# Kernel optimization log

Measured on AMD Instinct MI355X. Metric: run time of the kernel, lower is better.

## Reference

```python
import jax, jax.numpy as jnp
import numpy as np

NUM_TAGS = 48
START = 46
STOP = 47
B = 1024
S = 512
NEG_INF = -10000.0


def setup_inputs() -> dict:
    key = jax.random.key(0)
    k1, k2, k3, k4 = jax.random.split(key, 4)
    emissions = jax.random.normal(k1, (B, S, NUM_TAGS), dtype=jnp.float32)
    tags = jax.random.randint(k2, (B, S), 0, 46, dtype=jnp.int32)
    lengths = jax.random.randint(k3, (B,), S // 2, S + 1, dtype=jnp.int32)
    mask = (jnp.arange(S, dtype=jnp.int32)[None, :] < lengths[:, None]).astype(jnp.int32)
    # transitions parameter: uniform(-0.1, 0.1), then constraints from reset_parameters
    transitions = jax.random.uniform(k4, (NUM_TAGS, NUM_TAGS), dtype=jnp.float32,
                                     minval=-0.1, maxval=0.1)
    transitions = transitions.at[:, START].set(NEG_INF).at[STOP, :].set(NEG_INF)
    return {"emissions": emissions, "tags": tags, "mask": mask, "transitions": transitions}


def _log_sum_exp(x, axis):
    # matches torch helper: max + log(clamp(sum(exp(x - max)), 1e-10))
    m = jnp.max(x, axis=axis, keepdims=True)
    s = jnp.sum(jnp.exp(x - m), axis=axis, keepdims=True)
    return jnp.squeeze(m + jnp.log(jnp.clip(s, 1e-10)), axis=axis)


def _forward_alg(emissions, transitions, mask):
    b, s, t = emissions.shape
    alpha0 = jnp.full((b, t), NEG_INF, dtype=emissions.dtype).at[:, START].set(0.0)

    def step(alpha, xs):
        emit, m = xs  # emit: (B, T), m: (B,)
        # (B, prev, next)
        nxt = alpha[:, :, None] + transitions[None, :, :] + emit[:, None, :]
        alpha_t = _log_sum_exp(nxt, axis=1)
        alpha = jnp.where(m[:, None] > 0, alpha_t, alpha)
        return alpha, None

    alpha, _ = jax.lax.scan(step, alpha0,
                            (jnp.transpose(emissions, (1, 0, 2)), mask.T))
    terminal = alpha + transitions[STOP][None, :]
    return _log_sum_exp(terminal, axis=1)  # (B,)


def _score_sequence(emissions, transitions, tags, mask):
    b, s, _ = emissions.shape
    start_col = jnp.full((b, 1), START, dtype=tags.dtype)
    tws = jnp.concatenate([start_col, tags], axis=1)  # (B, S+1)
    # transitions[next, prev] per the original _score_sequence
    trans_sc = transitions[tws[:, 1:], tws[:, :-1]]  # (B, S)
    emit_sc = jnp.take_along_axis(emissions, tags[:, :, None].astype(jnp.int32), axis=2)[..., 0]
    score = jnp.sum((trans_sc + emit_sc) * mask.astype(emissions.dtype), axis=1)
    lengths = jnp.sum(mask, axis=1)
    last_tags = jnp.take_along_axis(tags, (lengths - 1)[:, None], axis=1)[:, 0]
    return score + transitions[STOP, last_tags]


def reference(emissions, tags, mask, transitions):
    log_z = _forward_alg(emissions, transitions, mask)
    gold = _score_sequence(emissions, transitions, tags, mask)
    return jnp.mean(log_z - gold)
```

## Files before the change

### kernel.cpp

```cpp
#include <hip/hip_runtime.h>
#include <hip/hip_bf16.h>
#include <stdint.h>
#include <math.h>

#define SLEN 512
#define NT 48
#define TAG_START 46
#define TAG_STOP 47

#define WS_QF 0
#define WS_WB 65536
#define WS_OUT 131072

#define B1OFF 1552

typedef __attribute__((ext_vector_type(8))) short bf16x8;
typedef __attribute__((ext_vector_type(4))) float f32x4;

typedef const uint32_t __attribute__((address_space(1)))* gptr_t;
typedef uint32_t __attribute__((address_space(3)))* lptr_t;

__device__ __forceinline__ void gload16(const float* g, float* l) {
  __builtin_amdgcn_global_load_lds((gptr_t)(uintptr_t)g, (lptr_t)(uintptr_t)l,
                                   16, 0, 0);
}
__device__ __forceinline__ uint32_t pk2(float a, float b) {
  return __builtin_amdgcn_perm(__float_as_uint(b), __float_as_uint(a),
                               0x07060302u);
}
__device__ __forceinline__ float fmax4(f32x4 v) {
  return fmaxf(fmaxf(v.x, v.y), fmaxf(v.z, v.w));
}

__global__ __launch_bounds__(64) void crf_split2_kernel(
    const float* __restrict__ em, const int* __restrict__ tags,
    const int* __restrict__ mask, const float* __restrict__ Tr,
    float* __restrict__ ws) {
  const int bid = blockIdx.x;
  const int dir = bid & 1;
  const int p = bid >> 1;
  const int b0 = 2 * p, b1 = 2 * p + 1;
  const int lane = threadIdx.x;
  const int g = lane >> 4;
  const int n = lane & 15;
  __shared__ __align__(16) float sbuf[2][B1OFF + 32 * NT];

  int len0, len1;
  {
    int lc0 = 0, lc1 = 0;
    const int* r0 = mask + (size_t)b0 * SLEN;
    const int* r1 = mask + (size_t)b1 * SLEN;
    for (int t = lane; t < SLEN; t += 64) {
      lc0 += r0[t];
      lc1 += r1[t];
    }
#pragma unroll
    for (int d = 32; d >= 1; d >>= 1) {
      lc0 += __shfl_xor(lc0, d);
      lc1 += __shfl_xor(lc1, d);
    }
    len0 = lc0;
    len1 = lc1;
  }
  const int m0 = len0 >> 1, m1 = len1 >> 1;
  const int st0 = dir ? (len0 - m0) : m0;
  const int st1 = dir ? (len1 - m1) : m1;
  const int smax = (st0 > st1) ? st0 : st1;
  const int my_st = (n == 0) ? st0 : ((n == 1) ? st1 : 0);

  bf16x8 A[3][2];
#pragma unroll
  for (int t = 0; t < 3; ++t) {
#pragma unroll
    for (int c = 0; c < 2; ++c) {
      union { uint32_t u[4]; bf16x8 v; } tmp;
#pragma unroll
      for (int ep = 0; ep < 4; ++ep) {
        float fe[2];
#pragma unroll
        for (int h = 0; h < 2; ++h) {
          const int e = 2 * ep + h;
          const int kl = (e < 4) ? (4 * g + e) : (16 + 4 * g + (e - 4));
          const int ig = 32 * c + kl;
          fe[h] = 0.0f;
          if (ig < NT)
            fe[h] = dir ? __expf(Tr[(16 * t + n) * NT + ig])
                        : __expf(Tr[ig * NT + 16 * t + n]);
        }
        tmp.u[ep] = pk2(fe[0], fe[1]);
      }
      A[t][c] = tmp.v;
    }
  }

  const f32x4 z4 = {0.f, 0.f, 0.f, 0.f};
  f32x4 v0 = z4, v1 = z4, v2 = z4;
  if (dir == 0) {
    if (n < 2 && g == 3) v2.z = 1.0f;
  } else {
    if (n < 2) {
      const f32x4 one4 = {1.f, 1.f, 1.f, 1.f};
      v0 = one4;
      v1 = one4;
      v2 = one4;
    }
  }
  int cbits = 0;
  f32x4 sv0 = z4, sv1 = z4, sv2 = z4;
  int scb = 0;

  const float* eb0 = em + (size_t)b0 * SLEN * NT;
  const float* eb1 = em + (size_t)b1 * SLEN * NT;
  const int myoff = (n == 1) ? B1OFF : 0;

  const int nwin = (smax + 31) >> 5;

  {
    const float* s0 = dir ? (eb0 + (size_t)(len0 - 32) * NT) : eb0;
    const float* s1 = dir ? (eb1 + (size_t)(len1 - 32) * NT) : eb1;
#pragma unroll
    for (int k = 0; k < 6; ++k) {
      gload16(s0 + k * 256 + lane * 4, &sbuf[0][k * 256]);
      gload16(s1 + k * 256 + lane * 4, &sbuf[0][B1OFF + k * 256]);
    }
  }

  float mxp = 1.0f;
  int rc = 0;

  for (int c = 0; c < nwin; ++c) {
    asm volatile("s_waitcnt vmcnt(0)" ::: "memory");
    if (c + 1 < nwin) {
      const float* s0 = dir ? (eb0 + (size_t)(len0 - 32 * (c + 2)) * NT)
                            : (eb0 + (size_t)(32 * (c + 1)) * NT);
      const float* s1 = dir ? (eb1 + (size_t)(len1 - 32 * (c + 2)) * NT)
                            : (eb1 + (size_t)(32 * (c + 1)) * NT);
#pragma unroll
      for (int k = 0; k < 6; ++k) {
        gload16(s0 + k * 256 + lane * 4, &sbuf[(c + 1) & 1][k * 256]);
        gload16(s1 + k * 256 + lane * 4, &sbuf[(c + 1) & 1][B1OFF + k * 256]);
      }
    }
    {
      float* base = &sbuf[c & 1][0];
#pragma unroll
      for (int r = 0; r < 6; ++r) {
        f32x4* pp = (f32x4*)(base + r * 256 + lane * 4);
        f32x4 vx = *pp;
        vx.x = __expf(vx.x);
        vx.y = __expf(vx.y);
        vx.z = __expf(vx.z);
        vx.w = __expf(vx.w);
        *pp = vx;
        f32x4* p2 = (f32x4*)(base + B1OFF + r * 256 + lane * 4);
        f32x4 vy = *p2;
        vy.x = __expf(vy.x);
        vy.y = __expf(vy.y);
        vy.z = __expf(vy.z);
        vy.w = __expf(vy.w);
        *p2 = vy;
      }
    }
    const int steps = (smax - 32 * c < 32) ? (smax - 32 * c) : 32;
    for (int sl = 0; sl < steps; ++sl) {
      const int s = 32 * c + sl;
      const int local = dir ? (31 - sl) : sl;
      const float* xb = &sbuf[c & 1][myoff + local * NT];
      const f32x4 x0 = *(const f32x4*)(xb + 4 * g);
      const f32x4 x1 = *(const f32x4*)(xb + 16 + 4 * g);
      const f32x4 x2 = *(const f32x4*)(xb + 32 + 4 * g);
      union { uint32_t u[4]; bf16x8 v; } B0, B1;
      if (dir == 0) {
        B0.u[0] = pk2(v0.x, v0.y);
        B0.u[1] = pk2(v0.z, v0.w);
        B0.u[2] = pk2(v1.x, v1.y);
        B0.u[3] = pk2(v1.z, v1.w);
        B1.u[0] = pk2(v2.x, v2.y);
        B1.u[1] = pk2(v2.z, v2.w);
        B1.u[2] = 0u;
        B1.u[3] = 0u;
      } else {
        const f32x4 y0 = v0 * x0, y1 = v1 * x1, y2 = v2 * x2;
        B0.u[0] = pk2(y0.x, y0.y);
        B0.u[1] = pk2(y0.z, y0.w);
        B0.u[2] = pk2(y1.x, y1.y);
        B0.u[3] = pk2(y1.z, y1.w);
        B1.u[0] = pk2(y2.x, y2.y);
        B1.u[1] = pk2(y2.z, y2.w);
        B1.u[2] = 0u;
        B1.u[3] = 0u;
      }
      f32x4 a0 = __builtin_amdgcn_mfma_f32_16x16x32_bf16(A[0][0], B0.v, z4, 0, 0, 0);
      f32x4 a1 = __builtin_amdgcn_mfma_f32_16x16x32_bf16(A[1][0], B0.v, z4, 0, 0, 0);
      f32x4 a2 = __builtin_amdgcn_mfma_f32_16x16x32_bf16(A[2][0], B0.v, z4, 0, 0, 0);
      a0 = __builtin_amdgcn_mfma_f32_16x16x32_bf16(A[0][1], B1.v, a0, 0, 0, 0);
      a1 = __builtin_amdgcn_mfma_f32_16x16x32_bf16(A[1][1], B1.v, a1, 0, 0, 0);
      a2 = __builtin_amdgcn_mfma_f32_16x16x32_bf16(A[2][1], B1.v, a2, 0, 0, 0);
      if (dir == 0) {
        v0 = a0 * x0;
        v1 = a1 * x1;
        v2 = a2 * x2;
      } else {
        v0 = a0;
        v1 = a1;
        v2 = a2;
      }
      ++rc;
      if (rc == 4) {
        float mx = fmaxf(fmax4(__builtin_elementwise_max(
                             __builtin_elementwise_max(v0, v1), v2)),
                         1e-30f);
        mx = fmaxf(mx, __shfl_xor(mx, 16));
        mx = fmaxf(mx, __shfl_xor(mx, 32));
        mxp = mx;
      } else if (rc == 6) {
        const int ex = ((__float_as_int(mxp) >> 23) & 255) - 126;
        const float sc = __int_as_float((127 - ex) << 23);
        v0 *= sc;
        v1 *= sc;
        v2 *= sc;
        cbits += ex;
        rc = 0;
      }
      if (s + 1 == st0 || s + 1 == st1) {
        const bool L = (n < 2) && (s + 1 == my_st);
        sv0 = L ? v0 : sv0;
        sv1 = L ? v1 : sv1;
        sv2 = L ? v2 : sv2;
        scb = L ? cbits : scb;
      }
    }
  }

  if (n < 2) {
    const int bb = n ? b1 : b0;
    float* dst = ws + (dir ? WS_WB : WS_QF) + (size_t)bb * 64;
    *(f32x4*)(dst + 4 * g) = sv0;
    *(f32x4*)(dst + 16 + 4 * g) = sv1;
    *(f32x4*)(dst + 32 + 4 * g) = sv2;
    if (g == 0) dst[48] = (float)scb;
  }

  if (dir == 0) {
#pragma unroll
    for (int which = 0; which < 2; ++which) {
      const int bb = which ? b1 : b0;
      const int ll = which ? len1 : len0;
      const float* eb = which ? eb1 : eb0;
      const int* trow = tags + (size_t)bb * SLEN;
      float gsc = 0.f;
      for (int t = lane; t < ll; t += 64) {
        const int tag = trow[t];
        const int prev = (t == 0) ? TAG_START : trow[t - 1];
        gsc += Tr[tag * NT + prev] + eb[(size_t)t * NT + tag];
      }
#pragma unroll
      for (int d = 32; d >= 1; d >>= 1) gsc += __shfl_xor(gsc, d);
      if (lane == 0) {
        const int last = trow[ll - 1];
        ws[WS_QF + (size_t)bb * 64 + 49] = gsc + Tr[TAG_STOP * NT + last];
      }
    }
  }
}

__global__ __launch_bounds__(64) void crf_combine_kernel(
    const float* __restrict__ Tr, float* __restrict__ ws) {
  const int b = blockIdx.x;
  const int lane = threadIdx.x;
  float p = 0.f;
  if (lane < NT)
    p = ws[WS_QF + (size_t)b * 64 + lane] * ws[WS_WB + (size_t)b * 64 + lane];
#pragma unroll
  for (int d = 32; d >= 1; d >>= 1) p += __shfl_xor(p, d);
  if (lane == 0) {
    const float cb =
        ws[WS_QF + (size_t)b * 64 + 48] + ws[WS_WB + (size_t)b * 64 + 48];
    const float gold = ws[WS_QF + (size_t)b * 64 + 49];
    ws[WS_OUT + b] =
        __logf(p) + cb * 0.69314718055994531f + Tr[TAG_STOP * NT] - gold;
  }
}

__global__ void crf_reduce_kernel(const float* __restrict__ wsrc,
                                  float* __restrict__ out, int nn) {
  const int tid = threadIdx.x;
  float v = (tid < nn) ? wsrc[tid] : 0.f;
#pragma unroll
  for (int d = 32; d >= 1; d >>= 1) v += __shfl_xor(v, d);
  __shared__ float part[16];
  if ((tid & 63) == 0) part[tid >> 6] = v;
  __syncthreads();
  if (tid == 0) {
    float s = 0.f;
    for (int i = 0; i < 16; ++i) s += part[i];
    out[0] = s / (float)nn;
  }
}

extern "C" void kernel_launch(void* const* d_in, const int* in_sizes, int n_in,
                              void* d_out, int out_size, void* d_ws, size_t ws_size,
                              hipStream_t stream) {
  const float* em = (const float*)d_in[0];
  const int* tags = (const int*)d_in[1];
  const int* mask = (const int*)d_in[2];
  const float* Tr = (const float*)d_in[3];
  const int B = in_sizes[0] / (SLEN * NT);

  float* ws = (float*)d_ws;
  crf_split2_kernel<<<B, 64, 0, stream>>>(em, tags, mask, Tr, ws);
  crf_combine_kernel<<<B, 64, 0, stream>>>(Tr, ws);
  crf_reduce_kernel<<<1, 1024, 0, stream>>>(ws + WS_OUT, (float*)d_out, B);
}
```

Before: 100.8 us.

## Align CRF split to multiples of 8 and unroll steps with per-group renormalization

Rounds the forward/backward split point and the backward start down to multiples of 8, handling the leftover tail rows of the backward pass in a short masked prologue that reads emissions directly from global memory. The main recurrence becomes an 8-way unrolled inner loop with one renormalization and one checkpoint capture per group, replacing the per-step counter, renorm branches and save checks. This removes per-step control overhead, at the cost of an extra prologue of up to 7 predicated steps and different renormalization timing, which could affect bf16 range safety.

```diff
diff --git a/kernel.cpp b/kernel.cpp
--- a/kernel.cpp
+++ b/kernel.cpp
@@ -30,6 +30,13 @@
 }
 __device__ __forceinline__ float fmax4(f32x4 v) {
   return fmaxf(fmaxf(v.x, v.y), fmaxf(v.z, v.w));
+}
+__device__ __forceinline__ f32x4 exp4(f32x4 v) {
+  v.x = __expf(v.x);
+  v.y = __expf(v.y);
+  v.z = __expf(v.z);
+  v.w = __expf(v.w);
+  return v;
 }
 
 __global__ __launch_bounds__(64) void crf_split2_kernel(
@@ -38,8 +45,8 @@
     float* __restrict__ ws) {
   const int bid = blockIdx.x;
   const int dir = bid & 1;
-  const int p = bid >> 1;
-  const int b0 = 2 * p, b1 = 2 * p + 1;
+  const int pr = bid >> 1;
+  const int b0 = 2 * pr, b1 = 2 * pr + 1;
   const int lane = threadIdx.x;
   const int g = lane >> 4;
   const int n = lane & 15;
@@ -62,11 +69,13 @@
     len0 = lc0;
     len1 = lc1;
   }
-  const int m0 = len0 >> 1, m1 = len1 >> 1;
-  const int st0 = dir ? (len0 - m0) : m0;
-  const int st1 = dir ? (len1 - m1) : m1;
-  const int smax = (st0 > st1) ? st0 : st1;
-  const int my_st = (n == 0) ? st0 : ((n == 1) ? st1 : 0);
+  const int m0 = (len0 >> 1) & ~7, m1 = (len1 >> 1) & ~7;
+  const int lp0 = len0 & ~7, lp1 = len1 & ~7;
+  const int p0 = len0 & 7, p1 = len1 & 7;
+  const int stm0 = dir ? (lp0 - m0) : m0;
+  const int stm1 = dir ? (lp1 - m1) : m1;
+  const int smax = (stm0 > stm1) ? stm0 : stm1;
+  const int my_stm = (n == 0) ? stm0 : ((n == 1) ? stm1 : -1);
 
   bf16x8 A[3][2];
 #pragma unroll
@@ -113,11 +122,87 @@
   const float* eb1 = em + (size_t)b1 * SLEN * NT;
   const int myoff = (n == 1) ? B1OFF : 0;
 
+  auto dostep_x = [&](f32x4 x0, f32x4 x1, f32x4 x2) {
+    union { uint32_t u[4]; bf16x8 v; } B0, B1;
+    if (dir == 0) {
+      B0.u[0] = pk2(v0.x, v0.y);
+      B0.u[1] = pk2(v0.z, v0.w);
+      B0.u[2] = pk2(v1.x, v1.y);
+      B0.u[3] = pk2(v1.z, v1.w);
+      B1.u[0] = pk2(v2.x, v2.y);
+      B1.u[1] = pk2(v2.z, v2.w);
+      B1.u[2] = 0u;
+      B1.u[3] = 0u;
+    } else {
+      const f32x4 y0 = v0 * x0, y1 = v1 * x1, y2 = v2 * x2;
+      B0.u[0] = pk2(y0.x, y0.y);
+      B0.u[1] = pk2(y0.z, y0.w);
+      B0.u[2] = pk2(y1.x, y1.y);
+      B0.u[3] = pk2(y1.z, y1.w);
+      B1.u[0] = pk2(y2.x, y2.y);
+      B1.u[1] = pk2(y2.z, y2.w);
+      B1.u[2] = 0u;
+      B1.u[3] = 0u;
+    }
+    f32x4 a0 = __builtin_amdgcn_mfma_f32_16x16x32_bf16(A[0][0], B0.v, z4, 0, 0, 0);
+    f32x4 a1 = __builtin_amdgcn_mfma_f32_16x16x32_bf16(A[1][0], B0.v, z4, 0, 0, 0);
+    f32x4 a2 = __builtin_amdgcn_mfma_f32_16x16x32_bf16(A[2][0], B0.v, z4, 0, 0, 0);
+    a0 = __builtin_amdgcn_mfma_f32_16x16x32_bf16(A[0][1], B1.v, a0, 0, 0, 0);
+    a1 = __builtin_amdgcn_mfma_f32_16x16x32_bf16(A[1][1], B1.v, a1, 0, 0, 0);
+    a2 = __builtin_amdgcn_mfma_f32_16x16x32_bf16(A[2][1], B1.v, a2, 0, 0, 0);
+    if (dir == 0) {
+      v0 = a0 * x0;
+      v1 = a1 * x1;
+      v2 = a2 * x2;
+    } else {
+      v0 = a0;
+      v1 = a1;
+      v2 = a2;
+    }
+  };
+  auto renorm = [&]() {
+    float mx = fmaxf(fmax4(__builtin_elementwise_max(
+                         __builtin_elementwise_max(v0, v1), v2)),
+                     1e-30f);
+    mx = fmaxf(mx, __shfl_xor(mx, 16));
+    mx = fmaxf(mx, __shfl_xor(mx, 32));
+    const int ex = ((__float_as_int(mx) >> 23) & 255) - 126;
+    const float sc = __int_as_float((127 - ex) << 23);
+    v0 *= sc;
+    v1 *= sc;
+    v2 *= sc;
+    cbits += ex;
+  };
+
+  if (dir == 1 && (p0 | p1)) {
+#pragma unroll
+    for (int k = 0; k < 7; ++k) {
+      const int i0 = k - (7 - p0);
+      const int i1 = k - (7 - p1);
+      int row0 = len0 - 1 - i0;
+      row0 = (row0 > len0 - 1) ? (len0 - 1) : row0;
+      int row1 = len1 - 1 - i1;
+      row1 = (row1 > len1 - 1) ? (len1 - 1) : row1;
+      const bool act = (n == 0) ? (i0 >= 0) : ((n == 1) ? (i1 >= 0) : false);
+      const int myrow = (n == 1) ? row1 : row0;
+      const float* rp = ((n == 1) ? eb1 : eb0) + (size_t)myrow * NT;
+      const f32x4 x0 = exp4(*(const f32x4*)(rp + 4 * g));
+      const f32x4 x1 = exp4(*(const f32x4*)(rp + 16 + 4 * g));
+      const f32x4 x2 = exp4(*(const f32x4*)(rp + 32 + 4 * g));
+      const f32x4 o0 = v0, o1 = v1, o2 = v2;
+      dostep_x(x0, x1, x2);
+      v0 = act ? v0 : o0;
+      v1 = act ? v1 : o1;
+      v2 = act ? v2 : o2;
+    }
+    renorm();
+  }
+
   const int nwin = (smax + 31) >> 5;
 
   {
-    const float* s0 = dir ? (eb0 + (size_t)(len0 - 32) * NT) : eb0;
-    const float* s1 = dir ? (eb1 + (size_t)(len1 - 32) * NT) : eb1;
+    const float* s0 = dir ? (eb0 + (size_t)(lp0 - 32) * NT) : eb0;
+    const float* s1 = dir ? (eb1 + (size_t)(lp1 - 32) * NT) : eb1;
 #pragma unroll
     for (int k = 0; k < 6; ++k) {
       gload16(s0 + k * 256 + lane * 4, &sbuf[0][k * 256]);
@@ -125,15 +210,12 @@
     }
   }
 
-  float mxp = 1.0f;
-  int rc = 0;
-
   for (int c = 0; c < nwin; ++c) {
     asm volatile("s_waitcnt vmcnt(0)" ::: "memory");
     if (c + 1 < nwin) {
-      const float* s0 = dir ? (eb0 + (size_t)(len0 - 32 * (c + 2)) * NT)
+      const float* s0 = dir ? (eb0 + (size_t)(lp0 - 32 * (c + 2)) * NT)
                             : (eb0 + (size_t)(32 * (c + 1)) * NT);
-      const float* s1 = dir ? (eb1 + (size_t)(len1 - 32 * (c + 2)) * NT)
+      const float* s1 = dir ? (eb1 + (size_t)(lp1 - 32 * (c + 2)) * NT)
                             : (eb1 + (size_t)(32 * (c + 1)) * NT);
 #pragma unroll
       for (int k = 0; k < 6; ++k) {
@@ -142,93 +224,35 @@
       }
     }
     {
-      float* base = &sbuf[c & 1][0];
+      float* base2 = &sbuf[c & 1][0];
 #pragma unroll
       for (int r = 0; r < 6; ++r) {
-        f32x4* pp = (f32x4*)(base + r * 256 + lane * 4);
-        f32x4 vx = *pp;
-        vx.x = __expf(vx.x);
-        vx.y = __expf(vx.y);
-        vx.z = __expf(vx.z);
-        vx.w = __expf(vx.w);
-        *pp = vx;
-        f32x4* p2 = (f32x4*)(base + B1OFF + r * 256 + lane * 4);
-        f32x4 vy = *p2;
-        vy.x = __expf(vy.x);
-        vy.y = __expf(vy.y);
-        vy.z = __expf(vy.z);
-        vy.w = __expf(vy.w);
-        *p2 = vy;
-      }
-    }
-    const int steps = (smax - 32 * c < 32) ? (smax - 32 * c) : 32;
-    for (int sl = 0; sl < steps; ++sl) {
-      const int s = 32 * c + sl;
-      const int local = dir ? (31 - sl) : sl;
-      const float* xb = &sbuf[c & 1][myoff + local * NT];
-      const f32x4 x0 = *(const f32x4*)(xb + 4 * g);
-      const f32x4 x1 = *(const f32x4*)(xb + 16 + 4 * g);
-      const f32x4 x2 = *(const f32x4*)(xb + 32 + 4 * g);
-      union { uint32_t u[4]; bf16x8 v; } B0, B1;
-      if (dir == 0) {
-        B0.u[0] = pk2(v0.x, v0.y);
-        B0.u[1] = pk2(v0.z, v0.w);
-        B0.u[2] = pk2(v1.x, v1.y);
-        B0.u[3] = pk2(v1.z, v1.w);
-        B1.u[0] = pk2(v2.x, v2.y);
-        B1.u[1] = pk2(v2.z, v2.w);
-        B1.u[2] = 0u;
-        B1.u[3] = 0u;
-      } else {
-        const f32x4 y0 = v0 * x0, y1 = v1 * x1, y2 = v2 * x2;
-        B0.u[0] = pk2(y0.x, y0.y);
-        B0.u[1] = pk2(y0.z, y0.w);
-        B0.u[2] = pk2(y1.x, y1.y);
-        B0.u[3] = pk2(y1.z, y1.w);
-        B1.u[0] = pk2(y2.x, y2.y);
-        B1.u[1] = pk2(y2.z, y2.w);
-        B1.u[2] = 0u;
-        B1.u[3] = 0u;
-      }
-      f32x4 a0 = __builtin_amdgcn_mfma_f32_16x16x32_bf16(A[0][0], B0.v, z4, 0, 0, 0);
-      f32x4 a1 = __builtin_amdgcn_mfma_f32_16x16x32_bf16(A[1][0], B0.v, z4, 0, 0, 0);
-      f32x4 a2 = __builtin_amdgcn_mfma_f32_16x16x32_bf16(A[2][0], B0.v, z4, 0, 0, 0);
-      a0 = __builtin_amdgcn_mfma_f32_16x16x32_bf16(A[0][1], B1.v, a0, 0, 0, 0);
-      a1 = __builtin_amdgcn_mfma_f32_16x16x32_bf16(A[1][1], B1.v, a1, 0, 0, 0);
-      a2 = __builtin_amdgcn_mfma_f32_16x16x32_bf16(A[2][1], B1.v, a2, 0, 0, 0);
-      if (dir == 0) {
-        v0 = a0 * x0;
-        v1 = a1 * x1;
-        v2 = a2 * x2;
-      } else {
-        v0 = a0;
-        v1 = a1;
-        v2 = a2;
-      }
-      ++rc;
-      if (rc == 4) {
-        float mx = fmaxf(fmax4(__builtin_elementwise_max(
-                             __builtin_elementwise_max(v0, v1), v2)),
-                         1e-30f);
-        mx = fmaxf(mx, __shfl_xor(mx, 16));
-        mx = fmaxf(mx, __shfl_xor(mx, 32));
-        mxp = mx;
-      } else if (rc == 6) {
-        const int ex = ((__float_as_int(mxp) >> 23) & 255) - 126;
-        const float sc = __int_as_float((127 - ex) << 23);
-        v0 *= sc;
-        v1 *= sc;
-        v2 *= sc;
-        cbits += ex;
-        rc = 0;
-      }
-      if (s + 1 == st0 || s + 1 == st1) {
-        const bool L = (n < 2) && (s + 1 == my_st);
-        sv0 = L ? v0 : sv0;
-        sv1 = L ? v1 : sv1;
-        sv2 = L ? v2 : sv2;
-        scb = L ? cbits : scb;
-      }
+        f32x4* pp = (f32x4*)(base2 + r * 256 + lane * 4);
+        *pp = exp4(*pp);
+        f32x4* p2 = (f32x4*)(base2 + B1OFF + r * 256 + lane * 4);
+        *p2 = exp4(*p2);
+      }
+    }
+    const float* wbase = &sbuf[c & 1][myoff];
+    const int base = 32 * c;
+    const int steps = (smax - base < 32) ? (smax - base) : 32;
+    const int ngr = steps >> 3;
+    for (int gi = 0; gi < ngr; ++gi) {
+      const int sl0 = gi << 3;
+#pragma unroll
+      for (int u = 0; u < 8; ++u) {
+        const int loc = dir ? (31 - (sl0 + u)) : (sl0 + u);
+        const float* xb = wbase + loc * NT;
+        dostep_x(*(const f32x4*)(xb + 4 * g), *(const f32x4*)(xb + 16 + 4 * g),
+                 *(const f32x4*)(xb + 32 + 4 * g));
+      }
+      renorm();
+      const int cnt = base + sl0 + 8;
+      const bool L = (n < 2) && (cnt == my_stm);
+      sv0 = L ? v0 : sv0;
+      sv1 = L ? v1 : sv1;
+      sv2 = L ? v2 : sv2;
+      scb = L ? cbits : scb;
     }
   }
 
```

New measurement: 84.42 us. 1.19x faster.
